# Kernel optimization log

Hardware: AMD Instinct MI355X
Metric: run time of the kernel (lower is better)

The kernel has to match this reference:

```python
import jax, jax.numpy as jnp
import numpy as np

N, E, G = 50000, 400000, 2000
H, HEADS, HD = 128, 4, 32


def setup_inputs() -> dict:
    key = jax.random.key(0)
    ks = jax.random.split(key, 16)
    nrm = lambda k, shape, s=0.05: jax.random.normal(k, shape, dtype=jnp.float32) * s
    inp = {}
    inp["x"] = jax.random.normal(ks[0], (N, 39), dtype=jnp.float32)
    inp["edge_index"] = jax.random.randint(ks[1], (2, E), 0, N, dtype=jnp.int32)
    inp["edge_attr"] = jax.random.normal(ks[2], (E, 8), dtype=jnp.float32)
    inp["batch"] = jnp.sort(jax.random.randint(ks[3], (N,), 0, G, dtype=jnp.int32))
    inp["in_W"] = nrm(ks[4], (39, H)); inp["in_b"] = jnp.zeros((H,), jnp.float32)
    inp["in_g"] = jnp.ones((H,), jnp.float32); inp["in_beta"] = jnp.zeros((H,), jnp.float32)
    inp["Wl"] = nrm(ks[5], (3, H, H)); inp["Wr"] = nrm(ks[6], (3, H, H))
    inp["We"] = nrm(ks[7], (3, 8, H)); inp["att"] = nrm(ks[8], (3, HEADS, HD))
    inp["conv_b"] = jnp.zeros((3, H), jnp.float32)
    inp["bn_g"] = jnp.ones((3, H), jnp.float32); inp["bn_b"] = jnp.zeros((3, H), jnp.float32)
    inp["t1_W"] = nrm(ks[9], (3 * H, 256)); inp["t1_b"] = jnp.zeros((256,), jnp.float32)
    inp["t1_g"] = jnp.ones((256,), jnp.float32); inp["t1_beta"] = jnp.zeros((256,), jnp.float32)
    inp["t2_W"] = nrm(ks[10], (256, 128)); inp["t2_b"] = jnp.zeros((128,), jnp.float32)
    inp["t2_g"] = jnp.ones((128,), jnp.float32); inp["t2_beta"] = jnp.zeros((128,), jnp.float32)
    inp["head_W"] = nrm(ks[11], (128, 12)); inp["head_b"] = jnp.zeros((12,), jnp.float32)
    return inp


def _bn(h, g, b):
    # BatchNorm1d in training mode: normalize with batch statistics.
    m = h.mean(0)
    v = ((h - m) ** 2).mean(0)
    return g * (h - m) * jax.lax.rsqrt(v + 1e-5) + b


def reference(x, edge_index, edge_attr, batch, in_W, in_b, in_g, in_beta,
              Wl, Wr, We, att, conv_b, bn_g, bn_b,
              t1_W, t1_b, t1_g, t1_beta, t2_W, t2_b, t2_g, t2_beta,
              head_W, head_b):
    src, dst = edge_index[0], edge_index[1]  # messages flow src -> dst (PyG convention)
    xn = jax.nn.relu(_bn(x @ in_W + in_b, in_g, in_beta))  # [N, H]
    for l in range(3):  # three residual GATv2 layers
        xl = (xn @ Wl[l]).reshape(N, HEADS, HD)  # lin_l (source transform)
        xr = (xn @ Wr[l]).reshape(N, HEADS, HD)  # lin_r (target transform)
        ep = (edge_attr @ We[l]).reshape(E, HEADS, HD)
        m = jax.nn.leaky_relu(xl[src] + xr[dst] + ep, 0.2)  # [E, HEADS, HD]
        alpha = jnp.einsum('ehd,hd->eh', m, att[l])  # [E, HEADS]
        amax = jax.ops.segment_max(alpha, dst, num_segments=N)
        amax = jnp.where(jnp.isfinite(amax), amax, 0.0)  # nodes with no in-edges
        ae = jnp.exp(alpha - amax[dst])
        denom = jax.ops.segment_sum(ae, dst, num_segments=N)
        a = ae / (denom[dst] + 1e-16)  # scatter-softmax over neighborhoods
        agg = jax.ops.segment_sum(xl[src] * a[:, :, None], dst, num_segments=N)
        h = agg.reshape(N, H) + conv_b[l]
        h = jax.nn.elu(_bn(h, bn_g[l], bn_b[l]))
        xn = xn + h
    # 3-way global pooling per graph
    cnt = jax.ops.segment_sum(jnp.ones((N,), jnp.float32), batch, num_segments=G)
    sadd = jax.ops.segment_sum(xn, batch, num_segments=G)
    smean = sadd / jnp.maximum(cnt, 1.0)[:, None]
    smax = jax.ops.segment_max(xn, batch, num_segments=G)
    smax = jnp.where(cnt[:, None] > 0, smax, 0.0)
    xg = jnp.concatenate([smean, smax, sadd], axis=1)  # [G, 3H]
    t = jax.nn.relu(_bn(xg @ t1_W + t1_b, t1_g, t1_beta))
    t = jax.nn.relu(_bn(t @ t2_W + t2_b, t2_g, t2_beta))
    return jax.nn.sigmoid(t @ head_W + head_b)  # [G, 12]
```

## Files before the change

### kernel.cpp

```cpp
#include <hip/hip_runtime.h>
#include <math.h>


constexpr int N_ = 50000;
constexpr int E_ = 400000;
constexpr int G_ = 2000;
constexpr int H_ = 128;
constexpr int IN_ = 39;

__global__ __launch_bounds__(256) void hist_kernel(const int* __restrict__ keys, int n,
                                                   int* __restrict__ cnt) {
  for (int i = blockIdx.x * 256 + threadIdx.x; i < n; i += gridDim.x * 256)
    atomicAdd(&cnt[keys[i]], 1);
}

__global__ __launch_bounds__(1024) void scan_excl4(const int* __restrict__ in,
                                                   int* __restrict__ out,
                                                   int* __restrict__ out2, int n) {
  __shared__ int wsum[16];
  __shared__ int carry_s, chunk_tot;
  int t = threadIdx.x, lane = t & 63, wid = t >> 6;
  if (t == 0) carry_s = 0;
  __syncthreads();
  for (int base = 0; base < n; base += 4096) {
    int idx = base + t * 4;
    int4 v = make_int4(0, 0, 0, 0);
    if (idx + 3 < n) {
      v = *(const int4*)&in[idx];
    } else {
      if (idx < n) v.x = in[idx];
      if (idx + 1 < n) v.y = in[idx + 1];
      if (idx + 2 < n) v.z = in[idx + 2];
      if (idx + 3 < n) v.w = in[idx + 3];
    }
    int tsum = v.x + v.y + v.z + v.w;
    int x = tsum;
#pragma unroll
    for (int off = 1; off < 64; off <<= 1) {
      int y = __shfl_up(x, off, 64);
      if (lane >= off) x += y;
    }
    if (lane == 63) wsum[wid] = x;
    __syncthreads();
    if (t == 0) {
      int acc = 0;
#pragma unroll
      for (int w = 0; w < 16; w++) { int tmp = wsum[w]; wsum[w] = acc; acc += tmp; }
      chunk_tot = acc;
    }
    __syncthreads();
    int b0 = carry_s + wsum[wid] + x - tsum;
    if (idx < n) { out[idx] = b0; out2[idx] = b0; }
    if (idx + 1 < n) { out[idx + 1] = b0 + v.x; out2[idx + 1] = b0 + v.x; }
    if (idx + 2 < n) { out[idx + 2] = b0 + v.x + v.y; out2[idx + 2] = b0 + v.x + v.y; }
    if (idx + 3 < n) { out[idx + 3] = b0 + v.x + v.y + v.z; out2[idx + 3] = b0 + v.x + v.y + v.z; }
    __syncthreads();
    if (t == 0) carry_s += chunk_tot;
    __syncthreads();
  }
  if (t == 0) out[n] = carry_s;
}

__global__ __launch_bounds__(256) void goff_from_sorted(const int* __restrict__ batch,
                                                        int* __restrict__ goff) {
  int i = blockIdx.x * 256 + threadIdx.x;
  if (i >= N_) return;
  int bi = batch[i];
  int bp = (i == 0) ? -1 : batch[i - 1];
  for (int g = bp + 1; g <= bi; g++) goff[g] = i;
  if (i == N_ - 1) {
    for (int g = bi + 1; g <= G_; g++) goff[g] = N_;
  }
}

__global__ __launch_bounds__(256) void edge_scatter(const int* __restrict__ ei,
                                                    const float* __restrict__ ea,
                                                    int* __restrict__ cursor,
                                                    int* __restrict__ esrc,
                                                    float* __restrict__ eas) {
  int e = blockIdx.x * 256 + threadIdx.x;
  if (e >= E_) return;
  int src = ei[e];
  int dst = ei[E_ + e];
  int j = atomicAdd(&cursor[dst], 1);
  esrc[j] = src;
  const float4* eav = (const float4*)(ea + (size_t)e * 8);
  float4* dstp = (float4*)(eas + (size_t)j * 8);
  dstp[0] = eav[0];
  dstp[1] = eav[1];
}

__global__ __launch_bounds__(256) void in_gemm(const float* __restrict__ x,
                                               const float* __restrict__ W,
                                               const float* __restrict__ b,
                                               float* __restrict__ y,
                                               float* __restrict__ ssum,
                                               float* __restrict__ ssq) {
  __shared__ float xs[32][40];
  __shared__ float s1[256], s2[256];
  int t = threadIdx.x;
  int row0 = blockIdx.x * 32;
  for (int i = t; i < 32 * IN_; i += 256) {
    int r = i / IN_, k = i % IN_;
    int row = row0 + r;
    xs[r][k] = (row < N_) ? x[row * IN_ + k] : 0.f;
  }
  __syncthreads();
  int col = t & 127;
  int half = t >> 7;
  float acc[16];
#pragma unroll
  for (int r = 0; r < 16; r++) acc[r] = 0.f;
  for (int k = 0; k < IN_; k++) {
    float w = W[k * H_ + col];
#pragma unroll
    for (int r = 0; r < 16; r++) acc[r] = fmaf(xs[half * 16 + r][k], w, acc[r]);
  }
  float bb = b[col];
  float a1 = 0.f, a2 = 0.f;
#pragma unroll
  for (int r = 0; r < 16; r++) {
    int row = row0 + half * 16 + r;
    float v = acc[r] + bb;
    if (row < N_) {
      y[row * H_ + col] = v;
      a1 += v;
      a2 = fmaf(v, v, a2);
    }
  }
  s1[t] = a1; s2[t] = a2;
  __syncthreads();
  if (t < 128) {
    atomicAdd(&ssum[t], s1[t] + s1[t + 128]);
    atomicAdd(&ssq[t], s2[t] + s2[t + 128]);
  }
}

template <int MODE>
__global__ __launch_bounds__(256) void gemm_xlxr(const float* __restrict__ xn_ro,
                                                 float* __restrict__ xn,
                                                 const float* __restrict__ buf,
                                                 const float* __restrict__ g,
                                                 const float* __restrict__ beta,
                                                 const float* __restrict__ mean,
                                                 const float* __restrict__ rstd,
                                                 const float* __restrict__ Wlp,
                                                 const float* __restrict__ Wrp,
                                                 float* __restrict__ xl,
                                                 float* __restrict__ xr) {
  __shared__ float xs[64][16];
  __shared__ float wl_s[16][128];
  __shared__ float wr_s[16][128];
  int t = threadIdx.x;
  int tx = t & 31;
  int ty = t >> 5;
  int row0 = blockIdx.x * 64;
  float4 accl[8], accr[8];
#pragma unroll
  for (int r = 0; r < 8; r++) {
    accl[r] = make_float4(0.f, 0.f, 0.f, 0.f);
    accr[r] = make_float4(0.f, 0.f, 0.f, 0.f);
  }
  for (int kc = 0; kc < H_; kc += 16) {
    __syncthreads();
    {
      int r = t >> 2;
      int k4 = (t & 3) * 4;
      int row = row0 + r;
      int c = kc + k4;
      float4 v = make_float4(0.f, 0.f, 0.f, 0.f);
      if (row < N_) {
        if (MODE == 0) {
          v = *(const float4*)&xn_ro[row * H_ + c];
        } else {
          float4 bv = *(const float4*)&buf[row * H_ + c];
          float4 gv = *(const float4*)&g[c];
          float4 be = *(const float4*)&beta[c];
          float4 mn = *(const float4*)&mean[c];
          float4 rs = *(const float4*)&rstd[c];
          float t0 = gv.x * (bv.x - mn.x) * rs.x + be.x;
          float t1 = gv.y * (bv.y - mn.y) * rs.y + be.y;
          float t2 = gv.z * (bv.z - mn.z) * rs.z + be.z;
          float t3 = gv.w * (bv.w - mn.w) * rs.w + be.w;
          if (MODE == 1) {
            v = make_float4(fmaxf(t0, 0.f), fmaxf(t1, 0.f), fmaxf(t2, 0.f), fmaxf(t3, 0.f));
          } else {
            float4 xo = *(const float4*)&xn[row * H_ + c];
            v.x = xo.x + ((t0 > 0.f) ? t0 : (__expf(t0) - 1.f));
            v.y = xo.y + ((t1 > 0.f) ? t1 : (__expf(t1) - 1.f));
            v.z = xo.z + ((t2 > 0.f) ? t2 : (__expf(t2) - 1.f));
            v.w = xo.w + ((t3 > 0.f) ? t3 : (__expf(t3) - 1.f));
          }
          *(float4*)&xn[row * H_ + c] = v;
        }
      }
      *(float4*)&xs[r][k4] = v;
    }
    for (int i = t; i < 512; i += 256) {
      int k = i >> 5;
      int c4 = (i & 31) * 4;
      *(float4*)&wl_s[k][c4] = *(const float4*)&Wlp[(kc + k) * H_ + c4];
      *(float4*)&wr_s[k][c4] = *(const float4*)&Wrp[(kc + k) * H_ + c4];
    }
    __syncthreads();
#pragma unroll
    for (int k = 0; k < 16; k += 4) {
      float4 xv[8];
#pragma unroll
      for (int r = 0; r < 8; r++) xv[r] = *(const float4*)&xs[ty * 8 + r][k];
#pragma unroll
      for (int kk = 0; kk < 4; kk++) {
        float4 wl = *(const float4*)&wl_s[k + kk][tx * 4];
        float4 wr = *(const float4*)&wr_s[k + kk][tx * 4];
#pragma unroll
        for (int r = 0; r < 8; r++) {
          float xvr = (kk == 0) ? xv[r].x : (kk == 1) ? xv[r].y : (kk == 2) ? xv[r].z : xv[r].w;
          accl[r].x = fmaf(xvr, wl.x, accl[r].x);
          accl[r].y = fmaf(xvr, wl.y, accl[r].y);
          accl[r].z = fmaf(xvr, wl.z, accl[r].z);
          accl[r].w = fmaf(xvr, wl.w, accl[r].w);
          accr[r].x = fmaf(xvr, wr.x, accr[r].x);
          accr[r].y = fmaf(xvr, wr.y, accr[r].y);
          accr[r].z = fmaf(xvr, wr.z, accr[r].z);
          accr[r].w = fmaf(xvr, wr.w, accr[r].w);
        }
      }
    }
  }
#pragma unroll
  for (int r = 0; r < 8; r++) {
    int row = row0 + ty * 8 + r;
    if (row < N_) {
      *(float4*)&xl[row * H_ + tx * 4] = accl[r];
      *(float4*)&xr[row * H_ + tx * 4] = accr[r];
    }
  }
}

__device__ __forceinline__ float ep8(const float4& a0, const float4& a1, const float* w) {
  float ep = a0.x * w[0];
  ep = fmaf(a0.y, w[1], ep);
  ep = fmaf(a0.z, w[2], ep);
  ep = fmaf(a0.w, w[3], ep);
  ep = fmaf(a1.x, w[4], ep);
  ep = fmaf(a1.y, w[5], ep);
  ep = fmaf(a1.z, w[6], ep);
  ep = fmaf(a1.w, w[7], ep);
  return ep;
}

__global__ __launch_bounds__(256) void agg_csr(const int* __restrict__ eoff,
                                               const int* __restrict__ esrc,
                                               const float* __restrict__ eas,
                                               const float* __restrict__ Wel,
                                               const float* __restrict__ attl,
                                               const float* __restrict__ xl,
                                               const float* __restrict__ xr,
                                               const float* __restrict__ cb,
                                               float* __restrict__ buf,
                                               float* __restrict__ ssum,
                                               float* __restrict__ ssq) {
  __shared__ float sA[256], sB[256], sC[256], sD[256];
  int t = threadIdx.x;
  int l = t & 63;
  int sub = t >> 6;
  int c0 = l * 2;
  float w0[8], w1[8];
#pragma unroll
  for (int k = 0; k < 8; k++) {
    float2 wv = *(const float2*)&Wel[k * H_ + c0];
    w0[k] = wv.x; w1[k] = wv.y;
  }
  float2 attv = *(const float2*)&attl[c0];
  float2 cbv = *(const float2*)&cb[c0];
  const float2* xl2 = (const float2*)xl;
  float a1_0 = 0.f, a1_1 = 0.f, a2_0 = 0.f, a2_1 = 0.f;
  for (int n = blockIdx.x * 4 + sub; n < N_; n += gridDim.x * 4) {
    float2 xrv = *(const float2*)&xr[n * H_ + c0];
    int e0 = eoff[n], e1 = eoff[n + 1];
    float acc0 = 0.f, acc1 = 0.f, den = 0.f;
    int j = e0;
    for (; j + 4 <= e1; j += 4) {
      int s0 = esrc[j], s1 = esrc[j + 1], s2 = esrc[j + 2], s3 = esrc[j + 3];
      const float4* ep = (const float4*)(eas + (size_t)j * 8);
      float4 a00 = ep[0], a01 = ep[1];
      float4 a10 = ep[2], a11 = ep[3];
      float4 a20 = ep[4], a21 = ep[5];
      float4 a30 = ep[6], a31 = ep[7];
      float2 x0 = xl2[(size_t)s0 * 64 + l];
      float2 x1 = xl2[(size_t)s1 * 64 + l];
      float2 x2 = xl2[(size_t)s2 * 64 + l];
      float2 x3 = xl2[(size_t)s3 * 64 + l];
      float m00 = x0.x + xrv.x + ep8(a00, a01, w0);
      float m01 = x0.y + xrv.y + ep8(a00, a01, w1);
      float m10 = x1.x + xrv.x + ep8(a10, a11, w0);
      float m11 = x1.y + xrv.y + ep8(a10, a11, w1);
      float m20 = x2.x + xrv.x + ep8(a20, a21, w0);
      float m21 = x2.y + xrv.y + ep8(a20, a21, w1);
      float m30 = x3.x + xrv.x + ep8(a30, a31, w0);
      float m31 = x3.y + xrv.y + ep8(a30, a31, w1);
      m00 = (m00 > 0.f) ? m00 : 0.2f * m00;
      m01 = (m01 > 0.f) ? m01 : 0.2f * m01;
      m10 = (m10 > 0.f) ? m10 : 0.2f * m10;
      m11 = (m11 > 0.f) ? m11 : 0.2f * m11;
      m20 = (m20 > 0.f) ? m20 : 0.2f * m20;
      m21 = (m21 > 0.f) ? m21 : 0.2f * m21;
      m30 = (m30 > 0.f) ? m30 : 0.2f * m30;
      m31 = (m31 > 0.f) ? m31 : 0.2f * m31;
      float p0 = fmaf(m00, attv.x, m01 * attv.y);
      float p1 = fmaf(m10, attv.x, m11 * attv.y);
      float p2 = fmaf(m20, attv.x, m21 * attv.y);
      float p3 = fmaf(m30, attv.x, m31 * attv.y);
#pragma unroll
      for (int off = 8; off > 0; off >>= 1) {
        p0 += __shfl_xor(p0, off, 64);
        p1 += __shfl_xor(p1, off, 64);
        p2 += __shfl_xor(p2, off, 64);
        p3 += __shfl_xor(p3, off, 64);
      }
      float e0v = __expf(p0), e1v = __expf(p1), e2v = __expf(p2), e3v = __expf(p3);
      acc0 = fmaf(e0v, x0.x, acc0); acc1 = fmaf(e0v, x0.y, acc1);
      acc0 = fmaf(e1v, x1.x, acc0); acc1 = fmaf(e1v, x1.y, acc1);
      acc0 = fmaf(e2v, x2.x, acc0); acc1 = fmaf(e2v, x2.y, acc1);
      acc0 = fmaf(e3v, x3.x, acc0); acc1 = fmaf(e3v, x3.y, acc1);
      den += (e0v + e1v) + (e2v + e3v);
    }
    for (; j < e1; j++) {
      int s0 = esrc[j];
      const float4* ep = (const float4*)(eas + (size_t)j * 8);
      float4 a00 = ep[0], a01 = ep[1];
      float2 x0 = xl2[(size_t)s0 * 64 + l];
      float m00 = x0.x + xrv.x + ep8(a00, a01, w0);
      float m01 = x0.y + xrv.y + ep8(a00, a01, w1);
      m00 = (m00 > 0.f) ? m00 : 0.2f * m00;
      m01 = (m01 > 0.f) ? m01 : 0.2f * m01;
      float p0 = fmaf(m00, attv.x, m01 * attv.y);
#pragma unroll
      for (int off = 8; off > 0; off >>= 1) p0 += __shfl_xor(p0, off, 64);
      float e0v = __expf(p0);
      acc0 = fmaf(e0v, x0.x, acc0);
      acc1 = fmaf(e0v, x0.y, acc1);
      den += e0v;
    }
    float inv = 1.f / (den + 1e-16f);
    float h0 = acc0 * inv + cbv.x;
    float h1 = acc1 * inv + cbv.y;
    *(float2*)&buf[n * H_ + c0] = make_float2(h0, h1);
    a1_0 += h0; a1_1 += h1;
    a2_0 = fmaf(h0, h0, a2_0); a2_1 = fmaf(h1, h1, a2_1);
  }
  sA[t] = a1_0; sB[t] = a1_1; sC[t] = a2_0; sD[t] = a2_1;
  __syncthreads();
  if (t < 64) {
    float r1 = sA[t] + sA[t + 64] + sA[t + 128] + sA[t + 192];
    float r2 = sB[t] + sB[t + 64] + sB[t + 128] + sB[t + 192];
    float r3 = sC[t] + sC[t + 64] + sC[t + 128] + sC[t + 192];
    float r4 = sD[t] + sD[t + 64] + sD[t + 128] + sD[t + 192];
    atomicAdd(&ssum[2 * t], r1);
    atomicAdd(&ssum[2 * t + 1], r2);
    atomicAdd(&ssq[2 * t], r3);
    atomicAdd(&ssq[2 * t + 1], r4);
  }
}

__global__ void bn_final(float* __restrict__ ssum, float* __restrict__ ssq, float rows_inv,
                         int cols, float* __restrict__ mean, float* __restrict__ rstd) {
  int c = threadIdx.x;
  if (c < cols) {
    float m = ssum[c] * rows_inv;
    float v = ssq[c] * rows_inv - m * m;
    mean[c] = m;
    rstd[c] = rsqrtf(v + 1e-5f);
    ssum[c] = 0.f;
    ssq[c] = 0.f;
  }
}

__global__ __launch_bounds__(256) void apply_bn_relu(const float* __restrict__ y,
                                                     float* __restrict__ out,
                                                     const float* __restrict__ g,
                                                     const float* __restrict__ beta,
                                                     const float* __restrict__ mean,
                                                     const float* __restrict__ rstd,
                                                     long total, int cmask) {
  long i = (long)blockIdx.x * 256 + threadIdx.x;
  if (i >= total) return;
  int c = (int)i & cmask;
  float v = g[c] * (y[i] - mean[c]) * rstd[c] + beta[c];
  out[i] = fmaxf(v, 0.f);
}

__global__ __launch_bounds__(256) void node_residual(float* __restrict__ xn,
                                                     const float* __restrict__ buf,
                                                     const float* __restrict__ g,
                                                     const float* __restrict__ beta,
                                                     const float* __restrict__ mean,
                                                     const float* __restrict__ rstd) {
  int i = blockIdx.x * 256 + threadIdx.x;
  if (i >= N_ * H_) return;
  int c = i & 127;
  float v = g[c] * (buf[i] - mean[c]) * rstd[c] + beta[c];
  v = (v > 0.f) ? v : (__expf(v) - 1.f);
  xn[i] += v;
}

__global__ __launch_bounds__(128) void pool_csr(const int* __restrict__ goff,
                                                const float* __restrict__ xn,
                                                float* __restrict__ xg) {
  int g = blockIdx.x;
  int t = threadIdx.x;
  int n0 = goff[g], n1 = goff[g + 1];
  float s = 0.f, mx = -INFINITY;
  for (int n = n0; n < n1; n++) {
    float v = xn[n * H_ + t];
    s += v;
    mx = fmaxf(mx, v);
  }
  float c = (float)(n1 - n0);
  xg[g * 384 + t] = s / fmaxf(c, 1.f);
  xg[g * 384 + 128 + t] = (c > 0.f) ? mx : 0.f;
  xg[g * 384 + 256 + t] = s;
}

template <int K, int COLS>
__global__ void mlp_gemm(const float* __restrict__ A, const float* __restrict__ W,
                         const float* __restrict__ b, float* __restrict__ Y, int rows,
                         float* __restrict__ ssum, float* __restrict__ ssq) {
  __shared__ float xs[8][K];
  int t = threadIdx.x;
  int row0 = blockIdx.x * 8;
  for (int i = t; i < 8 * K; i += COLS) {
    int r = i / K, k = i % K;
    int row = row0 + r;
    xs[r][k] = (row < rows) ? A[row * K + k] : 0.f;
  }
  __syncthreads();
  float acc[8];
#pragma unroll
  for (int r = 0; r < 8; r++) acc[r] = 0.f;
  for (int k = 0; k < K; k++) {
    float w = W[k * COLS + t];
#pragma unroll
    for (int r = 0; r < 8; r++) acc[r] = fmaf(xs[r][k], w, acc[r]);
  }
  float bb = b[t];
  float a1 = 0.f, a2 = 0.f;
#pragma unroll
  for (int r = 0; r < 8; r++) {
    int row = row0 + r;
    if (row < rows) {
      float v = acc[r] + bb;
      Y[row * COLS + t] = v;
      a1 += v;
      a2 = fmaf(v, v, a2);
    }
  }
  atomicAdd(&ssum[t], a1);
  atomicAdd(&ssq[t], a2);
}

__global__ __launch_bounds__(64) void head_kernel(const float* __restrict__ u,
                                                  const float* __restrict__ W,
                                                  const float* __restrict__ b,
                                                  float* __restrict__ out) {
  __shared__ float row[128];
  int g = blockIdx.x;
  int t = threadIdx.x;
  row[t] = u[g * 128 + t];
  row[t + 64] = u[g * 128 + 64 + t];
  __syncthreads();
  if (t < 12) {
    float acc = b[t];
    for (int k = 0; k < 128; k++) acc = fmaf(row[k], W[k * 12 + t], acc);
    out[g * 12 + t] = 1.f / (1.f + expf(-acc));
  }
}

extern "C" void kernel_launch(void* const* d_in, const int* in_sizes, int n_in, void* d_out,
                              int out_size, void* d_ws, size_t ws_size, hipStream_t stream) {
  (void)in_sizes; (void)n_in; (void)out_size; (void)ws_size;
  const float* x       = (const float*)d_in[0];
  const int*   ei      = (const int*)d_in[1];
  const float* ea      = (const float*)d_in[2];
  const int*   batch   = (const int*)d_in[3];
  const float* in_W    = (const float*)d_in[4];
  const float* in_b    = (const float*)d_in[5];
  const float* in_g    = (const float*)d_in[6];
  const float* in_beta = (const float*)d_in[7];
  const float* Wl      = (const float*)d_in[8];
  const float* Wr      = (const float*)d_in[9];
  const float* We      = (const float*)d_in[10];
  const float* att     = (const float*)d_in[11];
  const float* conv_b  = (const float*)d_in[12];
  const float* bn_g    = (const float*)d_in[13];
  const float* bn_b    = (const float*)d_in[14];
  const float* t1_W    = (const float*)d_in[15];
  const float* t1_b    = (const float*)d_in[16];
  const float* t1_g    = (const float*)d_in[17];
  const float* t1_beta = (const float*)d_in[18];
  const float* t2_W    = (const float*)d_in[19];
  const float* t2_b    = (const float*)d_in[20];
  const float* t2_g    = (const float*)d_in[21];
  const float* t2_beta = (const float*)d_in[22];
  const float* head_W  = (const float*)d_in[23];
  const float* head_b  = (const float*)d_in[24];
  float* out = (float*)d_out;

  float* p = (float*)d_ws;
  float* xn   = p; p += N_ * H_;
  float* xl   = p; p += N_ * H_;
  float* xr   = p; p += N_ * H_;
  float* buf  = p; p += N_ * H_;
  float* ssum = p; p += 256;
  float* ssq  = p; p += 256;
  float* mean = p; p += 256;
  float* rstd = p; p += 256;
  float* xg   = p; p += G_ * 384;
  float* u1   = p; p += G_ * 256;
  float* u2   = p; p += G_ * 128;
  float* eas  = p; p += (size_t)E_ * 8;
  int* ip = (int*)p;
  int* deg    = ip; ip += N_;
  int* eoff   = ip; ip += N_ + 1;
  int* cursor = ip; ip += N_;
  int* goff   = ip; ip += G_ + 1;
  int* esrc   = ip; ip += E_;

  hipMemsetAsync(deg, 0, (size_t)N_ * sizeof(int), stream);
  hist_kernel<<<1024, 256, 0, stream>>>(ei + E_, E_, deg);
  scan_excl4<<<1, 1024, 0, stream>>>(deg, eoff, cursor, N_);
  edge_scatter<<<(E_ + 255) / 256, 256, 0, stream>>>(ei, ea, cursor, esrc, eas);
  goff_from_sorted<<<(N_ + 255) / 256, 256, 0, stream>>>(batch, goff);

  hipMemsetAsync(ssum, 0, 512 * sizeof(float), stream);
  in_gemm<<<(N_ + 31) / 32, 256, 0, stream>>>(x, in_W, in_b, buf, ssum, ssq);
  bn_final<<<1, 256, 0, stream>>>(ssum, ssq, 1.f / N_, H_, mean, rstd);

  for (int l = 0; l < 3; l++) {
    if (l == 0) {
      gemm_xlxr<1><<<(N_ + 63) / 64, 256, 0, stream>>>(xn, xn, buf, in_g, in_beta, mean, rstd,
                                                       Wl + l * H_ * H_, Wr + l * H_ * H_, xl, xr);
    } else {
      gemm_xlxr<2><<<(N_ + 63) / 64, 256, 0, stream>>>(xn, xn, buf, bn_g + (l - 1) * H_,
                                                       bn_b + (l - 1) * H_, mean, rstd,
                                                       Wl + l * H_ * H_, Wr + l * H_ * H_, xl, xr);
    }
    agg_csr<<<2048, 256, 0, stream>>>(eoff, esrc, eas, We + l * 8 * H_, att + l * H_,
                                      xl, xr, conv_b + l * H_, buf, ssum, ssq);
    bn_final<<<1, 256, 0, stream>>>(ssum, ssq, 1.f / N_, H_, mean, rstd);
  }
  node_residual<<<25000, 256, 0, stream>>>(xn, buf, bn_g + 2 * H_, bn_b + 2 * H_, mean, rstd);
  pool_csr<<<G_, 128, 0, stream>>>(goff, xn, xg);

  mlp_gemm<384, 256><<<G_ / 8, 256, 0, stream>>>(xg, t1_W, t1_b, u1, G_, ssum, ssq);
  bn_final<<<1, 256, 0, stream>>>(ssum, ssq, 1.f / G_, 256, mean, rstd);
  apply_bn_relu<<<(G_ * 256 + 255) / 256, 256, 0, stream>>>(u1, u1, t1_g, t1_beta, mean, rstd,
                                                            (long)G_ * 256, 255);

  mlp_gemm<256, 128><<<G_ / 8, 128, 0, stream>>>(u1, t2_W, t2_b, u2, G_, ssum, ssq);
  bn_final<<<1, 256, 0, stream>>>(ssum, ssq, 1.f / G_, 128, mean, rstd);
  apply_bn_relu<<<(G_ * 128 + 255) / 256, 256, 0, stream>>>(u2, u2, t2_g, t2_beta, mean, rstd,
                                                            (long)G_ * 128, 127);

  head_kernel<<<G_, 64, 0, stream>>>(u2, head_W, head_b, out);
}
```

Before: 911.7 us.

## Store xl/xr and edge attrs in bf16, parallelize scan, fuse residual into pooling

Stores the xl/xr projections and the CSR-sorted edge attributes as packed bf16, halving the bytes gathered per edge in the aggregation kernel. The single-block prefix scan is replaced by a three-kernel multi-block scan. The final residual+ELU pass is fused into the per-graph pooling kernel, which saves a full N×H read and write. bn_final also now zeroes its accumulators for every thread. The trade-off is reduced precision in the attention logits and messages, plus two extra small kernel launches for the scan.

```diff
diff --git a/kernel.cpp b/kernel.cpp
--- a/kernel.cpp
+++ b/kernel.cpp
@@ -8,57 +8,70 @@
 constexpr int H_ = 128;
 constexpr int IN_ = 39;
 
+__device__ __forceinline__ unsigned pk_bf16(float a, float b) {
+  unsigned ua = __float_as_uint(a);
+  unsigned ub = __float_as_uint(b);
+  ua = (ua + 0x7fffu + ((ua >> 16) & 1u)) >> 16;
+  ub = (ub + 0x7fffu + ((ub >> 16) & 1u)) & 0xffff0000u;
+  return ua | ub;
+}
+__device__ __forceinline__ float up_lo(unsigned u) { return __uint_as_float(u << 16); }
+__device__ __forceinline__ float up_hi(unsigned u) { return __uint_as_float(u & 0xffff0000u); }
+
 __global__ __launch_bounds__(256) void hist_kernel(const int* __restrict__ keys, int n,
                                                    int* __restrict__ cnt) {
   for (int i = blockIdx.x * 256 + threadIdx.x; i < n; i += gridDim.x * 256)
     atomicAdd(&cnt[keys[i]], 1);
 }
 
-__global__ __launch_bounds__(1024) void scan_excl4(const int* __restrict__ in,
-                                                   int* __restrict__ out,
-                                                   int* __restrict__ out2, int n) {
+__global__ __launch_bounds__(1024) void scan_local(const int* __restrict__ in,
+                                                   int* __restrict__ outx,
+                                                   int* __restrict__ bsum, int n) {
   __shared__ int wsum[16];
-  __shared__ int carry_s, chunk_tot;
   int t = threadIdx.x, lane = t & 63, wid = t >> 6;
-  if (t == 0) carry_s = 0;
-  __syncthreads();
-  for (int base = 0; base < n; base += 4096) {
-    int idx = base + t * 4;
-    int4 v = make_int4(0, 0, 0, 0);
-    if (idx + 3 < n) {
-      v = *(const int4*)&in[idx];
-    } else {
-      if (idx < n) v.x = in[idx];
-      if (idx + 1 < n) v.y = in[idx + 1];
-      if (idx + 2 < n) v.z = in[idx + 2];
-      if (idx + 3 < n) v.w = in[idx + 3];
-    }
-    int tsum = v.x + v.y + v.z + v.w;
-    int x = tsum;
-#pragma unroll
-    for (int off = 1; off < 64; off <<= 1) {
-      int y = __shfl_up(x, off, 64);
-      if (lane >= off) x += y;
-    }
-    if (lane == 63) wsum[wid] = x;
-    __syncthreads();
-    if (t == 0) {
-      int acc = 0;
-#pragma unroll
-      for (int w = 0; w < 16; w++) { int tmp = wsum[w]; wsum[w] = acc; acc += tmp; }
-      chunk_tot = acc;
-    }
-    __syncthreads();
-    int b0 = carry_s + wsum[wid] + x - tsum;
-    if (idx < n) { out[idx] = b0; out2[idx] = b0; }
-    if (idx + 1 < n) { out[idx + 1] = b0 + v.x; out2[idx + 1] = b0 + v.x; }
-    if (idx + 2 < n) { out[idx + 2] = b0 + v.x + v.y; out2[idx + 2] = b0 + v.x + v.y; }
-    if (idx + 3 < n) { out[idx + 3] = b0 + v.x + v.y + v.z; out2[idx + 3] = b0 + v.x + v.y + v.z; }
-    __syncthreads();
-    if (t == 0) carry_s += chunk_tot;
-    __syncthreads();
-  }
-  if (t == 0) out[n] = carry_s;
+  int idx = blockIdx.x * 1024 + t;
+  int v = (idx < n) ? in[idx] : 0;
+  int x = v;
+#pragma unroll
+  for (int off = 1; off < 64; off <<= 1) {
+    int y = __shfl_up(x, off, 64);
+    if (lane >= off) x += y;
+  }
+  if (lane == 63) wsum[wid] = x;
+  __syncthreads();
+  if (t == 0) {
+    int acc = 0;
+#pragma unroll
+    for (int w = 0; w < 16; w++) { int tmp = wsum[w]; wsum[w] = acc; acc += tmp; }
+    bsum[blockIdx.x] = acc;
+  }
+  __syncthreads();
+  if (idx < n) outx[idx] = wsum[wid] + x - v;
+}
+
+__global__ __launch_bounds__(64) void scan_bsum(const int* __restrict__ bsum,
+                                                int* __restrict__ boff, int nb) {
+  int t = threadIdx.x;
+  int v = (t < nb) ? bsum[t] : 0;
+  int x = v;
+#pragma unroll
+  for (int off = 1; off < 64; off <<= 1) {
+    int y = __shfl_up(x, off, 64);
+    if (t >= off) x += y;
+  }
+  boff[t] = x - v;
+}
+
+__global__ __launch_bounds__(1024) void scan_add(int* __restrict__ eoff,
+                                                 const int* __restrict__ boff,
+                                                 int* __restrict__ cursor, int n) {
+  int idx = blockIdx.x * 1024 + threadIdx.x;
+  if (idx < n) {
+    int e = eoff[idx] + boff[idx >> 10];
+    eoff[idx] = e;
+    cursor[idx] = e;
+  }
+  if (idx == 0) eoff[n] = E_;
 }
 
 __global__ __launch_bounds__(256) void goff_from_sorted(const int* __restrict__ batch,
@@ -77,7 +90,7 @@
                                                     const float* __restrict__ ea,
                                                     int* __restrict__ cursor,
                                                     int* __restrict__ esrc,
-                                                    float* __restrict__ eas) {
+                                                    unsigned* __restrict__ easb) {
   int e = blockIdx.x * 256 + threadIdx.x;
   if (e >= E_) return;
   int src = ei[e];
@@ -85,9 +98,13 @@
   int j = atomicAdd(&cursor[dst], 1);
   esrc[j] = src;
   const float4* eav = (const float4*)(ea + (size_t)e * 8);
-  float4* dstp = (float4*)(eas + (size_t)j * 8);
-  dstp[0] = eav[0];
-  dstp[1] = eav[1];
+  float4 a0 = eav[0], a1 = eav[1];
+  uint4 o;
+  o.x = pk_bf16(a0.x, a0.y);
+  o.y = pk_bf16(a0.z, a0.w);
+  o.z = pk_bf16(a1.x, a1.y);
+  o.w = pk_bf16(a1.z, a1.w);
+  ((uint4*)easb)[j] = o;
 }
 
 __global__ __launch_bounds__(256) void in_gemm(const float* __restrict__ x,
@@ -146,8 +163,8 @@
                                                  const float* __restrict__ rstd,
                                                  const float* __restrict__ Wlp,
                                                  const float* __restrict__ Wrp,
-                                                 float* __restrict__ xl,
-                                                 float* __restrict__ xr) {
+                                                 unsigned* __restrict__ xlb,
+                                                 unsigned* __restrict__ xrb) {
   __shared__ float xs[64][16];
   __shared__ float wl_s[16][128];
   __shared__ float wr_s[16][128];
@@ -231,31 +248,36 @@
   for (int r = 0; r < 8; r++) {
     int row = row0 + ty * 8 + r;
     if (row < N_) {
-      *(float4*)&xl[row * H_ + tx * 4] = accl[r];
-      *(float4*)&xr[row * H_ + tx * 4] = accr[r];
-    }
-  }
-}
-
-__device__ __forceinline__ float ep8(const float4& a0, const float4& a1, const float* w) {
-  float ep = a0.x * w[0];
-  ep = fmaf(a0.y, w[1], ep);
-  ep = fmaf(a0.z, w[2], ep);
-  ep = fmaf(a0.w, w[3], ep);
-  ep = fmaf(a1.x, w[4], ep);
-  ep = fmaf(a1.y, w[5], ep);
-  ep = fmaf(a1.z, w[6], ep);
-  ep = fmaf(a1.w, w[7], ep);
+      uint2 ul, ur;
+      ul.x = pk_bf16(accl[r].x, accl[r].y);
+      ul.y = pk_bf16(accl[r].z, accl[r].w);
+      ur.x = pk_bf16(accr[r].x, accr[r].y);
+      ur.y = pk_bf16(accr[r].z, accr[r].w);
+      *(uint2*)&xlb[(size_t)row * 64 + tx * 2] = ul;
+      *(uint2*)&xrb[(size_t)row * 64 + tx * 2] = ur;
+    }
+  }
+}
+
+__device__ __forceinline__ float ep8u(const uint4& u, const float* w) {
+  float ep = up_lo(u.x) * w[0];
+  ep = fmaf(up_hi(u.x), w[1], ep);
+  ep = fmaf(up_lo(u.y), w[2], ep);
+  ep = fmaf(up_hi(u.y), w[3], ep);
+  ep = fmaf(up_lo(u.z), w[4], ep);
+  ep = fmaf(up_hi(u.z), w[5], ep);
+  ep = fmaf(up_lo(u.w), w[6], ep);
+  ep = fmaf(up_hi(u.w), w[7], ep);
   return ep;
 }
 
 __global__ __launch_bounds__(256) void agg_csr(const int* __restrict__ eoff,
                                                const int* __restrict__ esrc,
-                                               const float* __restrict__ eas,
+                                               const unsigned* __restrict__ easb,
                                                const float* __restrict__ Wel,
                                                const float* __restrict__ attl,
-                                               const float* __restrict__ xl,
-                                               const float* __restrict__ xr,
+                                               const unsigned* __restrict__ xlb,
+                                               const unsigned* __restrict__ xrb,
                                                const float* __restrict__ cb,
                                                float* __restrict__ buf,
                                                float* __restrict__ ssum,
@@ -273,32 +295,33 @@
   }
   float2 attv = *(const float2*)&attl[c0];
   float2 cbv = *(const float2*)&cb[c0];
-  const float2* xl2 = (const float2*)xl;
+  const uint4* eas4 = (const uint4*)easb;
   float a1_0 = 0.f, a1_1 = 0.f, a2_0 = 0.f, a2_1 = 0.f;
   for (int n = blockIdx.x * 4 + sub; n < N_; n += gridDim.x * 4) {
-    float2 xrv = *(const float2*)&xr[n * H_ + c0];
+    unsigned xru = xrb[(size_t)n * 64 + l];
+    float xr0 = up_lo(xru), xr1 = up_hi(xru);
     int e0 = eoff[n], e1 = eoff[n + 1];
     float acc0 = 0.f, acc1 = 0.f, den = 0.f;
     int j = e0;
     for (; j + 4 <= e1; j += 4) {
       int s0 = esrc[j], s1 = esrc[j + 1], s2 = esrc[j + 2], s3 = esrc[j + 3];
-      const float4* ep = (const float4*)(eas + (size_t)j * 8);
-      float4 a00 = ep[0], a01 = ep[1];
-      float4 a10 = ep[2], a11 = ep[3];
-      float4 a20 = ep[4], a21 = ep[5];
-      float4 a30 = ep[6], a31 = ep[7];
-      float2 x0 = xl2[(size_t)s0 * 64 + l];
-      float2 x1 = xl2[(size_t)s1 * 64 + l];
-      float2 x2 = xl2[(size_t)s2 * 64 + l];
-      float2 x3 = xl2[(size_t)s3 * 64 + l];
-      float m00 = x0.x + xrv.x + ep8(a00, a01, w0);
-      float m01 = x0.y + xrv.y + ep8(a00, a01, w1);
-      float m10 = x1.x + xrv.x + ep8(a10, a11, w0);
-      float m11 = x1.y + xrv.y + ep8(a10, a11, w1);
-      float m20 = x2.x + xrv.x + ep8(a20, a21, w0);
-      float m21 = x2.y + xrv.y + ep8(a20, a21, w1);
-      float m30 = x3.x + xrv.x + ep8(a30, a31, w0);
-      float m31 = x3.y + xrv.y + ep8(a30, a31, w1);
+      uint4 u0 = eas4[j], u1 = eas4[j + 1], u2 = eas4[j + 2], u3 = eas4[j + 3];
+      unsigned xu0 = xlb[(size_t)s0 * 64 + l];
+      unsigned xu1 = xlb[(size_t)s1 * 64 + l];
+      unsigned xu2 = xlb[(size_t)s2 * 64 + l];
+      unsigned xu3 = xlb[(size_t)s3 * 64 + l];
+      float x00 = up_lo(xu0), x01 = up_hi(xu0);
+      float x10 = up_lo(xu1), x11 = up_hi(xu1);
+      float x20 = up_lo(xu2), x21 = up_hi(xu2);
+      float x30 = up_lo(xu3), x31 = up_hi(xu3);
+      float m00 = x00 + xr0 + ep8u(u0, w0);
+      float m01 = x01 + xr1 + ep8u(u0, w1);
+      float m10 = x10 + xr0 + ep8u(u1, w0);
+      float m11 = x11 + xr1 + ep8u(u1, w1);
+      float m20 = x20 + xr0 + ep8u(u2, w0);
+      float m21 = x21 + xr1 + ep8u(u2, w1);
+      float m30 = x30 + xr0 + ep8u(u3, w0);
+      float m31 = x31 + xr1 + ep8u(u3, w1);
       m00 = (m00 > 0.f) ? m00 : 0.2f * m00;
       m01 = (m01 > 0.f) ? m01 : 0.2f * m01;
       m10 = (m10 > 0.f) ? m10 : 0.2f * m10;
@@ -319,33 +342,33 @@
         p3 += __shfl_xor(p3, off, 64);
       }
       float e0v = __expf(p0), e1v = __expf(p1), e2v = __expf(p2), e3v = __expf(p3);
-      acc0 = fmaf(e0v, x0.x, acc0); acc1 = fmaf(e0v, x0.y, acc1);
-      acc0 = fmaf(e1v, x1.x, acc0); acc1 = fmaf(e1v, x1.y, acc1);
-      acc0 = fmaf(e2v, x2.x, acc0); acc1 = fmaf(e2v, x2.y, acc1);
-      acc0 = fmaf(e3v, x3.x, acc0); acc1 = fmaf(e3v, x3.y, acc1);
+      acc0 = fmaf(e0v, x00, acc0); acc1 = fmaf(e0v, x01, acc1);
+      acc0 = fmaf(e1v, x10, acc0); acc1 = fmaf(e1v, x11, acc1);
+      acc0 = fmaf(e2v, x20, acc0); acc1 = fmaf(e2v, x21, acc1);
+      acc0 = fmaf(e3v, x30, acc0); acc1 = fmaf(e3v, x31, acc1);
       den += (e0v + e1v) + (e2v + e3v);
     }
     for (; j < e1; j++) {
       int s0 = esrc[j];
-      const float4* ep = (const float4*)(eas + (size_t)j * 8);
-      float4 a00 = ep[0], a01 = ep[1];
-      float2 x0 = xl2[(size_t)s0 * 64 + l];
-      float m00 = x0.x + xrv.x + ep8(a00, a01, w0);
-      float m01 = x0.y + xrv.y + ep8(a00, a01, w1);
+      uint4 u0 = eas4[j];
+      unsigned xu0 = xlb[(size_t)s0 * 64 + l];
+      float x00 = up_lo(xu0), x01 = up_hi(xu0);
+      float m00 = x00 + xr0 + ep8u(u0, w0);
+      float m01 = x01 + xr1 + ep8u(u0, w1);
       m00 = (m00 > 0.f) ? m00 : 0.2f * m00;
       m01 = (m01 > 0.f) ? m01 : 0.2f * m01;
       float p0 = fmaf(m00, attv.x, m01 * attv.y);
 #pragma unroll
       for (int off = 8; off > 0; off >>= 1) p0 += __shfl_xor(p0, off, 64);
       float e0v = __expf(p0);
-      acc0 = fmaf(e0v, x0.x, acc0);
-      acc1 = fmaf(e0v, x0.y, acc1);
+      acc0 = fmaf(e0v, x00, acc0);
+      acc1 = fmaf(e0v, x01, acc1);
       den += e0v;
     }
     float inv = 1.f / (den + 1e-16f);
     float h0 = acc0 * inv + cbv.x;
     float h1 = acc1 * inv + cbv.y;
-    *(float2*)&buf[n * H_ + c0] = make_float2(h0, h1);
+    *(float2*)&buf[(size_t)n * H_ + c0] = make_float2(h0, h1);
     a1_0 += h0; a1_1 += h1;
     a2_0 = fmaf(h0, h0, a2_0); a2_1 = fmaf(h1, h1, a2_1);
   }
@@ -371,9 +394,9 @@
     float v = ssq[c] * rows_inv - m * m;
     mean[c] = m;
     rstd[c] = rsqrtf(v + 1e-5f);
-    ssum[c] = 0.f;
-    ssq[c] = 0.f;
-  }
+  }
+  ssum[c] = 0.f;
+  ssq[c] = 0.f;
 }
 
 __global__ __launch_bounds__(256) void apply_bn_relu(const float* __restrict__ y,
@@ -390,36 +413,30 @@
   out[i] = fmaxf(v, 0.f);
 }
 
-__global__ __launch_bounds__(256) void node_residual(float* __restrict__ xn,
+__global__ __launch_bounds__(128) void pool_residual(const int* __restrict__ goff,
+                                                     const float* __restrict__ xn,
                                                      const float* __restrict__ buf,
                                                      const float* __restrict__ g,
                                                      const float* __restrict__ beta,
                                                      const float* __restrict__ mean,
-                                                     const float* __restrict__ rstd) {
-  int i = blockIdx.x * 256 + threadIdx.x;
-  if (i >= N_ * H_) return;
-  int c = i & 127;
-  float v = g[c] * (buf[i] - mean[c]) * rstd[c] + beta[c];
-  v = (v > 0.f) ? v : (__expf(v) - 1.f);
-  xn[i] += v;
-}
-
-__global__ __launch_bounds__(128) void pool_csr(const int* __restrict__ goff,
-                                                const float* __restrict__ xn,
-                                                float* __restrict__ xg) {
-  int g = blockIdx.x;
-  int t = threadIdx.x;
-  int n0 = goff[g], n1 = goff[g + 1];
+                                                     const float* __restrict__ rstd,
+                                                     float* __restrict__ xg) {
+  int gr = blockIdx.x;
+  int t = threadIdx.x;
+  int n0 = goff[gr], n1 = goff[gr + 1];
+  float gg = g[t], bb = beta[t], mm = mean[t], rr = rstd[t];
   float s = 0.f, mx = -INFINITY;
   for (int n = n0; n < n1; n++) {
-    float v = xn[n * H_ + t];
+    float w = gg * (buf[(size_t)n * H_ + t] - mm) * rr + bb;
+    w = (w > 0.f) ? w : (__expf(w) - 1.f);
+    float v = xn[(size_t)n * H_ + t] + w;
     s += v;
     mx = fmaxf(mx, v);
   }
   float c = (float)(n1 - n0);
-  xg[g * 384 + t] = s / fmaxf(c, 1.f);
-  xg[g * 384 + 128 + t] = (c > 0.f) ? mx : 0.f;
-  xg[g * 384 + 256 + t] = s;
+  xg[gr * 384 + t] = s / fmaxf(c, 1.f);
+  xg[gr * 384 + 128 + t] = (c > 0.f) ? mx : 0.f;
+  xg[gr * 384 + 256 + t] = s;
 }
 
 template <int K, int COLS>
@@ -508,8 +525,6 @@
 
   float* p = (float*)d_ws;
   float* xn   = p; p += N_ * H_;
-  float* xl   = p; p += N_ * H_;
-  float* xr   = p; p += N_ * H_;
   float* buf  = p; p += N_ * H_;
   float* ssum = p; p += 256;
   float* ssq  = p; p += 256;
@@ -518,18 +533,25 @@
   float* xg   = p; p += G_ * 384;
   float* u1   = p; p += G_ * 256;
   float* u2   = p; p += G_ * 128;
-  float* eas  = p; p += (size_t)E_ * 8;
-  int* ip = (int*)p;
+  unsigned* up = (unsigned*)p;
+  unsigned* xlb  = up; up += (size_t)N_ * 64;
+  unsigned* xrb  = up; up += (size_t)N_ * 64;
+  unsigned* easb = up; up += (size_t)E_ * 4;
+  int* ip = (int*)up;
   int* deg    = ip; ip += N_;
   int* eoff   = ip; ip += N_ + 1;
   int* cursor = ip; ip += N_;
   int* goff   = ip; ip += G_ + 1;
   int* esrc   = ip; ip += E_;
+  int* bsum   = ip; ip += 64;
+  int* boff   = ip; ip += 64;
 
   hipMemsetAsync(deg, 0, (size_t)N_ * sizeof(int), stream);
   hist_kernel<<<1024, 256, 0, stream>>>(ei + E_, E_, deg);
-  scan_excl4<<<1, 1024, 0, stream>>>(deg, eoff, cursor, N_);
-  edge_scatter<<<(E_ + 255) / 256, 256, 0, stream>>>(ei, ea, cursor, esrc, eas);
+  scan_local<<<49, 1024, 0, stream>>>(deg, eoff, bsum, N_);
+  scan_bsum<<<1, 64, 0, stream>>>(bsum, boff, 49);
+  scan_add<<<49, 1024, 0, stream>>>(eoff, boff, cursor, N_);
+  edge_scatter<<<(E_ + 255) / 256, 256, 0, stream>>>(ei, ea, cursor, esrc, easb);
   goff_from_sorted<<<(N_ + 255) / 256, 256, 0, stream>>>(batch, goff);
 
   hipMemsetAsync(ssum, 0, 512 * sizeof(float), stream);
@@ -539,18 +561,21 @@
   for (int l = 0; l < 3; l++) {
     if (l == 0) {
       gemm_xlxr<1><<<(N_ + 63) / 64, 256, 0, stream>>>(xn, xn, buf, in_g, in_beta, mean, rstd,
-                                                       Wl + l * H_ * H_, Wr + l * H_ * H_, xl, xr);
+                                                       Wl + l * H_ * H_, Wr + l * H_ * H_,
+                                                       xlb, xrb);
     } else {
       gemm_xlxr<2><<<(N_ + 63) / 64, 256, 0, stream>>>(xn, xn, buf, bn_g + (l - 1) * H_,
                                                        bn_b + (l - 1) * H_, mean, rstd,
-                                                       Wl + l * H_ * H_, Wr + l * H_ * H_, xl, xr);
-    }
-    agg_csr<<<2048, 256, 0, stream>>>(eoff, esrc, eas, We + l * 8 * H_, att + l * H_,
-                                      xl, xr, conv_b + l * H_, buf, ssum, ssq);
+                                                       Wl + l * H_ * H_, Wr + l * H_ * H_,
+                                                       xlb, xrb);
+    }
+    agg_csr<<<2048, 256, 0, stream>>>(eoff, esrc, easb, We + l * 8 * H_, att + l * H_,
+                                      xlb, xrb, conv_b + l * H_, buf, ssum, ssq);
     bn_final<<<1, 256, 0, stream>>>(ssum, ssq, 1.f / N_, H_, mean, rstd);
   }
-  node_residual<<<25000, 256, 0, stream>>>(xn, buf, bn_g + 2 * H_, bn_b + 2 * H_, mean, rstd);
-  pool_csr<<<G_, 128, 0, stream>>>(goff, xn, xg);
+
+  pool_residual<<<G_, 128, 0, stream>>>(goff, xn, buf, bn_g + 2 * H_, bn_b + 2 * H_,
+                                        mean, rstd, xg);
 
   mlp_gemm<384, 256><<<G_ / 8, 256, 0, stream>>>(xg, t1_W, t1_b, u1, G_, ssum, ssq);
   bn_final<<<1, 256, 0, stream>>>(ssum, ssq, 1.f / G_, 256, mean, rstd);
```

New measurement: 881.2 us. 3.3% less time.
